# Optimization experiments

Hardware: AMD Instinct MI355X
Metric: run time of the kernel (lower is better)

The kernel has to match this reference:

```python
import jax, jax.numpy as jnp
import numpy as np

B, L, H = 4096, 4096, 1024  # batch, num_labels, hidden_size


def setup_inputs() -> dict:
    key = jax.random.key(0)
    k1, k2, k3, k4, k5 = jax.random.split(key, 5)
    return {
        "bert_output": jax.random.normal(k1, (B, H), dtype=jnp.float32),
        "label_embed": jax.random.normal(k2, (L, H), dtype=jnp.float32),
        "W": jax.random.normal(k3, (L, H), dtype=jnp.float32) * 0.02,
        "b": jax.random.normal(k4, (L,), dtype=jnp.float32) * 0.02,
        "labels": jax.random.randint(k5, (B, L), 0, 2, dtype=jnp.int32),
    }


def reference(bert_output, label_embed, W, b, labels):
    # Original: output[i, j] = classifier(bert_output[i] + label_embed[j])[j]
    #         = sum_k (x[i,k] + E[j,k]) * W[j,k] + b[j]
    #         = (x @ W^T)[i,j] + (E * W).sum(-1)[j] + b[j]
    xWt = jnp.einsum('bh,lh->bl', bert_output, W)          # [B, L] GEMM
    diag_bias = jnp.sum(label_embed * W, axis=-1) + b       # [L] epilogue
    logits = xWt + diag_bias[None, :]                       # [B, L]
    return logits
```

## Files before the change

kernel.cpp:

```cpp
#include <hip/hip_runtime.h>
#include <hip/hip_bf16.h>

#define Bdim 4096
#define Ldim 4096
#define Hdim 1024
#define BM 256
#define BN 256
#define BK 64
#define NT (Hdim / BK)

typedef __attribute__((ext_vector_type(8))) __bf16 bf16x8;
typedef __attribute__((ext_vector_type(4))) float floatx4;

__device__ __forceinline__ unsigned short f2bf(float f) {
  union { __hip_bfloat16 h; unsigned short u; } c;
  c.h = __float2bfloat16(f);
  return c.u;
}

__global__ __launch_bounds__(256) void prep_kernel(
    const float* __restrict__ X, const float* __restrict__ E,
    const float* __restrict__ W, const float* __restrict__ b,
    unsigned short* __restrict__ Xb, unsigned short* __restrict__ Wb,
    float* __restrict__ bias) {
  const int blk = blockIdx.x;
  const int t = threadIdx.x;
  if (blk < Ldim) {
    const int row = blk;
    const float4 wv = reinterpret_cast<const float4*>(W + (size_t)row * Hdim)[t];
    const float4 ev = reinterpret_cast<const float4*>(E + (size_t)row * Hdim)[t];
    ushort4 o;
    o.x = f2bf(wv.x); o.y = f2bf(wv.y); o.z = f2bf(wv.z); o.w = f2bf(wv.w);
    reinterpret_cast<ushort4*>(Wb + (size_t)row * Hdim)[t] = o;
    float dot = wv.x * ev.x + wv.y * ev.y + wv.z * ev.z + wv.w * ev.w;
#pragma unroll
    for (int off = 32; off > 0; off >>= 1) dot += __shfl_down(dot, off, 64);
    __shared__ float part[4];
    if ((t & 63) == 0) part[t >> 6] = dot;
    __syncthreads();
    if (t == 0) bias[row] = part[0] + part[1] + part[2] + part[3] + b[row];
  } else {
    const int i = (blk - Ldim) * 256 + t;
    float4 v = reinterpret_cast<const float4*>(X)[i];
    ushort4 o;
    o.x = f2bf(v.x); o.y = f2bf(v.y); o.z = f2bf(v.z); o.w = f2bf(v.w);
    reinterpret_cast<ushort4*>(Xb)[i] = o;
  }
}

__global__ __launch_bounds__(512) void gemm_bias_kernel(
    const unsigned short* __restrict__ A,
    const unsigned short* __restrict__ Bw,
    const float* __restrict__ bias,
    float* __restrict__ C) {
  static_assert(NT >= 3, "pipeline needs >=3 K-tiles");
  __shared__ __align__(16) unsigned short lds[2][2][BM * BK];

  const int tid = threadIdx.x;
  const int wave = tid >> 6;
  const int lane = tid & 63;
  const int wm = wave >> 2;
  const int wn = wave & 3;
  const int m_blk = blockIdx.y * BM;
  const int n_blk = blockIdx.x * BN;

  const int srow = wave * 8 + (lane >> 3);
  const int skofs = ((lane & 7) ^ (lane >> 3)) * 8;
  const unsigned short* gA = A + (size_t)(m_blk + srow) * Hdim + skofs;
  const unsigned short* gB = Bw + (size_t)(n_blk + srow) * Hdim + skofs;

  const int fr = lane & 15;
  const int fq = lane >> 4;
  const int kx0 = ((fq) ^ (fr & 7)) * 8;
  const int kx1 = ((4 + fq) ^ (fr & 7)) * 8;
  const int aBase = (wm * 128 + fr) * BK;
  const int bBase = (wn * 64 + fr) * BK;

  floatx4 acc[8][4] = {};
  bf16x8 af[8][2], bfv[4][2];

#define GLL(src, dst)                                                  \
  __builtin_amdgcn_global_load_lds(                                    \
      (const __attribute__((address_space(1))) void*)(src),            \
      (__attribute__((address_space(3))) void*)(dst), 16, 0, 0)

#define STAGE1(c, mat, j, kt)                                          \
  do {                                                                 \
    const unsigned short* _g = (mat) ? gB : gA;                        \
    GLL(_g + (size_t)((j) * 128) * Hdim + (size_t)(kt) * 64,           \
        &lds[c][mat][((j) * 128 + wave * 8) * BK]);                    \
    GLL(_g + (size_t)((j) * 128 + 64) * Hdim + (size_t)(kt) * 64,      \
        &lds[c][mat][((j) * 128 + 64 + wave * 8) * BK]);               \
  } while (0)

#define READ_R1(c)                                                     \
  do {                                                                 \
    _Pragma("unroll") for (int mi = 0; mi < 4; ++mi) {                 \
      af[mi][0] = *(const bf16x8*)&lds[c][0][aBase + mi * 16 * BK + kx0]; \
      af[mi][1] = *(const bf16x8*)&lds[c][0][aBase + mi * 16 * BK + kx1]; \
    }                                                                  \
    _Pragma("unroll") for (int ni = 0; ni < 2; ++ni) {                 \
      bfv[ni][0] = *(const bf16x8*)&lds[c][1][bBase + ni * 16 * BK + kx0]; \
      bfv[ni][1] = *(const bf16x8*)&lds[c][1][bBase + ni * 16 * BK + kx1]; \
    }                                                                  \
  } while (0)

#define READ_R2(c)                                                     \
  do {                                                                 \
    _Pragma("unroll") for (int mi = 4; mi < 8; ++mi) {                 \
      af[mi][0] = *(const bf16x8*)&lds[c][0][aBase + mi * 16 * BK + kx0]; \
      af[mi][1] = *(const bf16x8*)&lds[c][0][aBase + mi * 16 * BK + kx1]; \
    }                                                                  \
    _Pragma("unroll") for (int ni = 2; ni < 4; ++ni) {                 \
      bfv[ni][0] = *(const bf16x8*)&lds[c][1][bBase + ni * 16 * BK + kx0]; \
      bfv[ni][1] = *(const bf16x8*)&lds[c][1][bBase + ni * 16 * BK + kx1]; \
    }                                                                  \
  } while (0)

#define MFMA_Q(M0, N0)                                                 \
  do {                                                                 \
    __builtin_amdgcn_s_setprio(1);                                     \
    _Pragma("unroll") for (int mi = (M0); mi < (M0) + 4; ++mi)         \
      _Pragma("unroll") for (int ni = (N0); ni < (N0) + 2; ++ni) {     \
        acc[mi][ni] = __builtin_amdgcn_mfma_f32_16x16x32_bf16(         \
            af[mi][0], bfv[ni][0], acc[mi][ni], 0, 0, 0);              \
        acc[mi][ni] = __builtin_amdgcn_mfma_f32_16x16x32_bf16(         \
            af[mi][1], bfv[ni][1], acc[mi][ni], 0, 0, 0);              \
      }                                                                \
    __builtin_amdgcn_s_setprio(0);                                     \
  } while (0)

  STAGE1(0, 0, 0, 0);
  STAGE1(0, 0, 1, 0);
  STAGE1(0, 1, 0, 0);
  STAGE1(0, 1, 1, 0);
  STAGE1(1, 0, 0, 1);

#pragma unroll 1
  for (int t = 0; t < NT - 1; ++t) {
    const int c = t & 1;
    STAGE1(c ^ 1, 0, 1, t + 1);
    asm volatile("s_waitcnt vmcnt(4)\n\ts_barrier" ::: "memory");
    READ_R1(c);
    MFMA_Q(0, 0);
    STAGE1(c ^ 1, 1, 0, t + 1);
    READ_R2(c);
    MFMA_Q(4, 2);
    asm volatile("s_barrier" ::: "memory");
    STAGE1(c ^ 1, 1, 1, t + 1);
    MFMA_Q(0, 2);
    if (t < NT - 2) STAGE1(c, 0, 0, t + 2);
    MFMA_Q(4, 0);
  }

  asm volatile("s_waitcnt vmcnt(0)\n\ts_barrier" ::: "memory");
  READ_R1(1);
  READ_R2(1);
  MFMA_Q(0, 0);
  MFMA_Q(4, 2);
  MFMA_Q(0, 2);
  MFMA_Q(4, 0);

#undef GLL
#undef STAGE1
#undef READ_R1
#undef READ_R2
#undef MFMA_Q

  const int col0 = n_blk + wn * 64 + fr;
  const int row0 = m_blk + wm * 128 + fq * 4;
#pragma unroll
  for (int ni = 0; ni < 4; ++ni) {
    const float bs = bias[col0 + ni * 16];
#pragma unroll
    for (int mi = 0; mi < 8; ++mi) {
      float* cp = C + (size_t)(row0 + mi * 16) * Ldim + (col0 + ni * 16);
      floatx4 v = acc[mi][ni];
      cp[0 * (size_t)Ldim] = v.x + bs;
      cp[1 * (size_t)Ldim] = v.y + bs;
      cp[2 * (size_t)Ldim] = v.z + bs;
      cp[3 * (size_t)Ldim] = v.w + bs;
    }
  }
}

extern "C" void kernel_launch(void* const* d_in, const int* in_sizes, int n_in,
                              void* d_out, int out_size, void* d_ws, size_t ws_size,
                              hipStream_t stream) {
  const float* X = (const float*)d_in[0];
  const float* E = (const float*)d_in[1];
  const float* W = (const float*)d_in[2];
  const float* b = (const float*)d_in[3];
  float* out = (float*)d_out;

  unsigned short* Xb = (unsigned short*)d_ws;
  unsigned short* Wb = Xb + (size_t)Bdim * Hdim;
  float* bias = (float*)(Wb + (size_t)Ldim * Hdim);

  prep_kernel<<<Ldim + Bdim, 256, 0, stream>>>(X, E, W, b, Xb, Wb, bias);
  dim3 grid(Ldim / BN, Bdim / BM);
  gemm_bias_kernel<<<grid, 512, 0, stream>>>(Xb, Wb, bias, out);
}
```

Before: 52.39 us.

## Reschedule GEMM main loop into barrier-separated read/MFMA phases with occupancy hint

```diff
diff --git a/kernel.cpp b/kernel.cpp
--- a/kernel.cpp
+++ b/kernel.cpp
@@ -48,7 +48,7 @@
   }
 }
 
-__global__ __launch_bounds__(512) void gemm_bias_kernel(
+__global__ __launch_bounds__(512, 2) void gemm_bias_kernel(
     const unsigned short* __restrict__ A,
     const unsigned short* __restrict__ Bw,
     const float* __restrict__ bias,
@@ -93,25 +93,17 @@
         &lds[c][mat][((j) * 128 + 64 + wave * 8) * BK]);               \
   } while (0)
 
-#define READ_R1(c)                                                     \
-  do {                                                                 \
-    _Pragma("unroll") for (int mi = 0; mi < 4; ++mi) {                 \
+#define READ_A(c, lo)                                                  \
+  do {                                                                 \
+    _Pragma("unroll") for (int mi = (lo); mi < (lo) + 4; ++mi) {       \
       af[mi][0] = *(const bf16x8*)&lds[c][0][aBase + mi * 16 * BK + kx0]; \
       af[mi][1] = *(const bf16x8*)&lds[c][0][aBase + mi * 16 * BK + kx1]; \
     }                                                                  \
-    _Pragma("unroll") for (int ni = 0; ni < 2; ++ni) {                 \
-      bfv[ni][0] = *(const bf16x8*)&lds[c][1][bBase + ni * 16 * BK + kx0]; \
-      bfv[ni][1] = *(const bf16x8*)&lds[c][1][bBase + ni * 16 * BK + kx1]; \
-    }                                                                  \
-  } while (0)
-
-#define READ_R2(c)                                                     \
-  do {                                                                 \
-    _Pragma("unroll") for (int mi = 4; mi < 8; ++mi) {                 \
-      af[mi][0] = *(const bf16x8*)&lds[c][0][aBase + mi * 16 * BK + kx0]; \
-      af[mi][1] = *(const bf16x8*)&lds[c][0][aBase + mi * 16 * BK + kx1]; \
-    }                                                                  \
-    _Pragma("unroll") for (int ni = 2; ni < 4; ++ni) {                 \
+  } while (0)
+
+#define READ_B(c, lo)                                                  \
+  do {                                                                 \
+    _Pragma("unroll") for (int ni = (lo); ni < (lo) + 2; ++ni) {       \
       bfv[ni][0] = *(const bf16x8*)&lds[c][1][bBase + ni * 16 * BK + kx0]; \
       bfv[ni][1] = *(const bf16x8*)&lds[c][1][bBase + ni * 16 * BK + kx1]; \
     }                                                                  \
@@ -130,42 +122,65 @@
     __builtin_amdgcn_s_setprio(0);                                     \
   } while (0)
 
+#define BAR __builtin_amdgcn_s_barrier()
+#define LGKM0 asm volatile("s_waitcnt lgkmcnt(0)" ::: "memory")
+
   STAGE1(0, 0, 0, 0);
   STAGE1(0, 0, 1, 0);
   STAGE1(0, 1, 0, 0);
   STAGE1(0, 1, 1, 0);
   STAGE1(1, 0, 0, 1);
+  asm volatile("s_waitcnt vmcnt(2)\n\ts_barrier" ::: "memory");
 
 #pragma unroll 1
   for (int t = 0; t < NT - 1; ++t) {
     const int c = t & 1;
     STAGE1(c ^ 1, 0, 1, t + 1);
-    asm volatile("s_waitcnt vmcnt(4)\n\ts_barrier" ::: "memory");
-    READ_R1(c);
+    STAGE1(c ^ 1, 1, 0, t + 1);
+    READ_A(c, 0);
+    READ_B(c, 0);
+    BAR;
+    LGKM0;
     MFMA_Q(0, 0);
-    STAGE1(c ^ 1, 1, 0, t + 1);
-    READ_R2(c);
+    BAR;
+    STAGE1(c ^ 1, 1, 1, t + 1);
+    READ_A(c, 4);
+    BAR;
+    LGKM0;
+    MFMA_Q(4, 0);
+    BAR;
+    READ_B(c, 2);
+    BAR;
+    LGKM0;
+    MFMA_Q(0, 2);
+    BAR;
+    if (t < NT - 2) {
+      STAGE1(c, 0, 0, t + 2);
+      asm volatile("s_waitcnt vmcnt(2)\n\ts_barrier" ::: "memory");
+    } else {
+      asm volatile("s_waitcnt vmcnt(0)\n\ts_barrier" ::: "memory");
+    }
     MFMA_Q(4, 2);
-    asm volatile("s_barrier" ::: "memory");
-    STAGE1(c ^ 1, 1, 1, t + 1);
-    MFMA_Q(0, 2);
-    if (t < NT - 2) STAGE1(c, 0, 0, t + 2);
-    MFMA_Q(4, 0);
+    BAR;
   }
 
-  asm volatile("s_waitcnt vmcnt(0)\n\ts_barrier" ::: "memory");
-  READ_R1(1);
-  READ_R2(1);
+  READ_A(1, 0);
+  READ_B(1, 0);
+  READ_A(1, 4);
+  READ_B(1, 2);
+  LGKM0;
   MFMA_Q(0, 0);
+  MFMA_Q(4, 0);
+  MFMA_Q(0, 2);
   MFMA_Q(4, 2);
-  MFMA_Q(0, 2);
-  MFMA_Q(4, 0);
 
 #undef GLL
 #undef STAGE1
-#undef READ_R1
-#undef READ_R2
+#undef READ_A
+#undef READ_B
 #undef MFMA_Q
+#undef BAR
+#undef LGKM0
 
   const int col0 = n_blk + wn * 64 + fr;
   const int row0 = m_blk + wm * 128 + fq * 4;
```

Measured after the change: 55.79 us. 6.5% more time.
